# Optimization experiments

Hardware: AMD Instinct MI355X
Metric: run time of the kernel (lower is better)

The kernel has to match this reference:

```python
import jax, jax.numpy as jnp
import numpy as np

DIM = 1024
NUM_HEADS = 16
HEAD_DIM = DIM // NUM_HEADS
GATE_HID = DIM // 4


def setup_inputs() -> dict:
    key = jax.random.key(0)
    ks = jax.random.split(key, 16)
    B, S, D = 2, 2048, DIM
    sc = 1.0 / np.sqrt(D)
    inp = {
        "h": jax.random.normal(ks[0], (B, S, D), jnp.float32),
        "x": jax.random.normal(ks[1], (B, S, D), jnp.float32),
        # attention projections, stored (in, out) so y = x @ W + b
        "Wq": jax.random.normal(ks[2], (D, D), jnp.float32) * sc,
        "bq": jnp.zeros((D,), jnp.float32),
        "Wk": jax.random.normal(ks[3], (D, D), jnp.float32) * sc,
        "bk": jnp.zeros((D,), jnp.float32),
        "Wv": jax.random.normal(ks[4], (D, D), jnp.float32) * sc,
        "bv": jnp.zeros((D,), jnp.float32),
        "Wo": jax.random.normal(ks[5], (D, D), jnp.float32) * sc,
        "bo": jnp.zeros((D,), jnp.float32),
        # gating MLP: Linear(2D -> D//4) -> GELU -> Linear(D//4 -> D) -> sigmoid
        "Wg1": jax.random.normal(ks[6], (2 * D, GATE_HID), jnp.float32) * (1.0 / np.sqrt(2 * D)),
        "bg1": jnp.zeros((GATE_HID,), jnp.float32),
        "Wg2": jax.random.normal(ks[7], (GATE_HID, D), jnp.float32) * (1.0 / np.sqrt(GATE_HID)),
        "bg2": jnp.zeros((D,), jnp.float32),
    }
    return inp


def reference(h, x, Wq, bq, Wk, bk, Wv, bv, Wo, bo, Wg1, bg1, Wg2, bg2):
    B, S, D = h.shape
    # gated blend of latent h and input x
    gate_in = jnp.concatenate([h, x], axis=-1)                      # (B,S,2D)
    gate = jax.nn.sigmoid((jax.nn.gelu(gate_in @ Wg1 + bg1, approximate=False)) @ Wg2 + bg2)
    blended = gate * h + (1.0 - gate) * x                           # (B,S,D)
    # multi-head self-attention
    q = (blended @ Wq + bq).reshape(B, S, NUM_HEADS, HEAD_DIM)
    k = (blended @ Wk + bk).reshape(B, S, NUM_HEADS, HEAD_DIM)
    v = (blended @ Wv + bv).reshape(B, S, NUM_HEADS, HEAD_DIM)
    scale = 1.0 / np.sqrt(HEAD_DIM).astype(np.float32)
    scores = jnp.einsum('bqhd,bkhd->bhqk', q, k) * scale            # (B,H,S,S)
    attn = jax.nn.softmax(scores, axis=-1)
    out = jnp.einsum('bhqk,bkhd->bqhd', attn, v).reshape(B, S, D)
    return out @ Wo + bo
```

## Files before the change

kernel.cpp:

```cpp
#include <hip/hip_runtime.h>
#include <hip/hip_bf16.h>


typedef __attribute__((ext_vector_type(4))) unsigned int u32x4;
typedef __attribute__((ext_vector_type(8))) short s16x8;
typedef __attribute__((ext_vector_type(8))) unsigned short u16x8;
typedef __attribute__((ext_vector_type(4))) unsigned short u16x4;
typedef __attribute__((ext_vector_type(4))) float f32x4;

#define QSCALE 0.18033688011112043f
#define DEFER_THR 11.54f

__device__ __forceinline__ unsigned short f2bf(float f) {
    unsigned int i = __builtin_bit_cast(unsigned int, f);
    i += 0x7FFFu + ((i >> 16) & 1u);
    return (unsigned short)(i >> 16);
}

__device__ __forceinline__ void gload16(const void* g, void* l) {
    __builtin_amdgcn_global_load_lds(
        (const __attribute__((address_space(1))) void*)g,
        (__attribute__((address_space(3))) void*)l, 16, 0, 0);
}

struct TEntry { const float* src; unsigned short* dst; int K; int N; };
struct TTable { TEntry e[6]; };

__global__ __launch_bounds__(256) void transpose_cvt_all(TTable tt)
{
    const TEntry E = tt.e[blockIdx.y];
    const int ntn = E.N >> 5;
    if ((int)blockIdx.x >= (E.K >> 5) * ntn) return;
    const int n0 = ((int)blockIdx.x % ntn) * 32, k0 = ((int)blockIdx.x / ntn) * 32;
    __shared__ float tile[32][33];
    const int tx = threadIdx.x & 31, ty = threadIdx.x >> 5;
#pragma unroll
    for (int i = 0; i < 4; ++i)
        tile[ty + i * 8][tx] = E.src[(size_t)(k0 + ty + i * 8) * E.N + n0 + tx];
    __syncthreads();
#pragma unroll
    for (int i = 0; i < 4; ++i)
        E.dst[(size_t)(n0 + ty + i * 8) * E.K + k0 + tx] = f2bf(tile[tx][ty + i * 8]);
}

__global__ __launch_bounds__(256) void build_hx(
    const float* __restrict__ h, const float* __restrict__ x,
    unsigned short* __restrict__ hx)
{
    const int idx = blockIdx.x * 256 + threadIdx.x;
    const size_t e = (size_t)idx * 8;
    const int r = (int)(e >> 11), c = (int)(e & 2047);
    const float* src = (c < 1024) ? (h + (size_t)r * 1024 + c)
                                  : (x + (size_t)r * 1024 + (c - 1024));
    u16x8 o;
#pragma unroll
    for (int j = 0; j < 8; ++j) o[j] = f2bf(src[j]);
    *reinterpret_cast<u16x8*>(hx + e) = o;
}

__global__ __launch_bounds__(256) void concat_bias(
    const float* __restrict__ bq, const float* __restrict__ bk,
    const float* __restrict__ bv, float* __restrict__ dst)
{
    const int i = blockIdx.x * 256 + threadIdx.x;
    if (i < 1024) dst[i] = bq[i];
    else if (i < 2048) dst[i] = bk[i - 1024];
    else if (i < 3072) dst[i] = bv[i - 2048];
}

__global__ __launch_bounds__(256) void transpose_v(
    const unsigned short* __restrict__ qkv, unsigned short* __restrict__ vt)
{
    __shared__ unsigned short t[64][65];
    const int st = blockIdx.x;
    const int bh = blockIdx.y;
    const int b = bh >> 4, h = bh & 15;
    const int tx = threadIdx.x & 63, ty = threadIdx.x >> 6;
    const int s0 = st * 64;
    const size_t base = (size_t)(b * 2048 + s0) * 3072 + 2048 + h * 64;
#pragma unroll
    for (int i = 0; i < 16; ++i)
        t[ty + i * 4][tx] = qkv[base + (size_t)(ty + i * 4) * 3072 + tx];
    __syncthreads();
    const size_t obase = (size_t)(bh * 64) * 2048 + s0;
#pragma unroll
    for (int i = 0; i < 16; ++i)
        vt[obase + (size_t)(ty + i * 4) * 2048 + tx] = t[tx][ty + i * 4];
}

enum { EPI_GELU = 1, EPI_BLEND = 2, EPI_F32 = 3, EPI_QKV = 4 };

template <int EPI>
__global__ __launch_bounds__(256, 2) void gemm_kernel(
    const unsigned short* __restrict__ A, int lda,
    const unsigned short* __restrict__ Bt, int ldb,
    const float* __restrict__ bias,
    void* __restrict__ Cv, int ldc, int K,
    const float* __restrict__ hb, const float* __restrict__ xb,
    int swzn, int ntn)
{
    __shared__ unsigned short Alds[2][128 * 32];
    __shared__ unsigned short Blds[2][128 * 32];

    const int tid = threadIdx.x;
    const int lane = tid & 63;
    const int w = tid >> 6;
    const int wr = w >> 1, wc = w & 1;
    int mt, nt;
    if (swzn > 0) {
        const int xcd = (int)blockIdx.x & 7, seq = (int)blockIdx.x >> 3;
        nt = xcd * swzn + seq % swzn;
        mt = seq / swzn;
    } else {
        nt = (int)blockIdx.x % ntn;
        mt = (int)blockIdx.x / ntn;
    }
    const int m0 = mt * 128, n0 = nt * 128;
    const int lrow = lane & 15, lko = (lane >> 4) * 8;

    const int grow = w * 32 + (lane >> 2);
    const int gk8 = (lane & 3) * 8;
    const unsigned short* ga0 = A + (size_t)(m0 + grow) * lda + gk8;
    const unsigned short* ga1 = ga0 + (size_t)16 * lda;
    const unsigned short* gb0 = Bt + (size_t)(n0 + grow) * ldb + gk8;
    const unsigned short* gb1 = gb0 + (size_t)16 * ldb;

    auto stage = [&](int buf, int k0) {
        unsigned short* la = &Alds[buf][w * 1024];
        unsigned short* lb = &Blds[buf][w * 1024];
        gload16(ga0 + k0, la);
        gload16(ga1 + k0, la + 512);
        gload16(gb0 + k0, lb);
        gload16(gb1 + k0, lb + 512);
    };

    f32x4 acc[4][4];
#pragma unroll
    for (int i = 0; i < 4; ++i)
#pragma unroll
        for (int j = 0; j < 4; ++j) acc[i][j] = (f32x4){0.f, 0.f, 0.f, 0.f};

    const int kks = K >> 5;
    stage(0, 0);
    __syncthreads();

    for (int t = 0; t < kks; ++t) {
        const int cur = t & 1;
        if (t + 1 < kks) stage(cur ^ 1, (t + 1) << 5);

        s16x8 af[4], bfr[4];
#pragma unroll
        for (int mi = 0; mi < 4; ++mi)
            af[mi] = *reinterpret_cast<const s16x8*>(&Alds[cur][(wr * 64 + mi * 16 + lrow) * 32 + lko]);
#pragma unroll
        for (int ni = 0; ni < 4; ++ni)
            bfr[ni] = *reinterpret_cast<const s16x8*>(&Blds[cur][(wc * 64 + ni * 16 + lrow) * 32 + lko]);
#pragma unroll
        for (int mi = 0; mi < 4; ++mi)
#pragma unroll
            for (int ni = 0; ni < 4; ++ni)
                acc[mi][ni] = __builtin_amdgcn_mfma_f32_16x16x32_bf16(af[mi], bfr[ni], acc[mi][ni], 0, 0, 0);

        __syncthreads();
    }

    const int rbase = m0 + wr * 64;
    const int cbase = n0 + wc * 64;
#pragma unroll
    for (int mi = 0; mi < 4; ++mi) {
#pragma unroll
        for (int j = 0; j < 4; ++j) {
            const int r = rbase + mi * 16 + (lane >> 4) * 4 + j;
#pragma unroll
            for (int ni = 0; ni < 4; ++ni) {
                const int c = cbase + ni * 16 + (lane & 15);
                float v = acc[mi][ni][j] + bias[c];
                if constexpr (EPI == EPI_GELU) {
                    float g = 0.5f * v * (1.f + erff(v * 0.70710678118654752f));
                    ((unsigned short*)Cv)[(size_t)r * ldc + c] = f2bf(g);
                } else if constexpr (EPI == EPI_BLEND) {
                    float gate = 1.f / (1.f + __expf(-v));
                    const size_t o = (size_t)r * ldc + c;
                    float bl = gate * hb[o] + (1.f - gate) * xb[o];
                    ((unsigned short*)Cv)[o] = f2bf(bl);
                } else if constexpr (EPI == EPI_QKV) {
                    const float scl = (c < 1024) ? QSCALE : 1.f;
                    ((unsigned short*)Cv)[(size_t)r * ldc + c] = f2bf(v * scl);
                } else {
                    ((float*)Cv)[(size_t)r * ldc + c] = v;
                }
            }
        }
    }
}

__global__ __launch_bounds__(256, 2) void gemm_gelu64(
    const unsigned short* __restrict__ A, int lda,
    const unsigned short* __restrict__ Bt, int ldb,
    const float* __restrict__ bias,
    unsigned short* __restrict__ C, int ldc, int K)
{
    __shared__ unsigned short Alds[2][64 * 32];
    __shared__ unsigned short Blds[2][64 * 32];

    const int tid = threadIdx.x;
    const int lane = tid & 63;
    const int w = tid >> 6;
    const int wr = w >> 1, wc = w & 1;
    const int nt = (int)blockIdx.x & 3, mt = (int)blockIdx.x >> 2;
    const int m0 = mt * 64, n0 = nt * 64;
    const int lrow = lane & 15, lko = (lane >> 4) * 8;

    const int grow = w * 16 + (lane >> 2);
    const int gk8 = (lane & 3) * 8;
    const unsigned short* ga = A + (size_t)(m0 + grow) * lda + gk8;
    const unsigned short* gb = Bt + (size_t)(n0 + grow) * ldb + gk8;

    auto stage = [&](int buf, int k0) {
        gload16(ga + k0, &Alds[buf][w * 512]);
        gload16(gb + k0, &Blds[buf][w * 512]);
    };

    f32x4 acc[2][2];
#pragma unroll
    for (int i = 0; i < 2; ++i)
#pragma unroll
        for (int j = 0; j < 2; ++j) acc[i][j] = (f32x4){0.f, 0.f, 0.f, 0.f};

    const int kks = K >> 5;
    stage(0, 0);
    __syncthreads();

    for (int t = 0; t < kks; ++t) {
        const int cur = t & 1;
        if (t + 1 < kks) stage(cur ^ 1, (t + 1) << 5);

        s16x8 af[2], bfr[2];
#pragma unroll
        for (int mi = 0; mi < 2; ++mi)
            af[mi] = *reinterpret_cast<const s16x8*>(&Alds[cur][(wr * 32 + mi * 16 + lrow) * 32 + lko]);
#pragma unroll
        for (int ni = 0; ni < 2; ++ni)
            bfr[ni] = *reinterpret_cast<const s16x8*>(&Blds[cur][(wc * 32 + ni * 16 + lrow) * 32 + lko]);
#pragma unroll
        for (int mi = 0; mi < 2; ++mi)
#pragma unroll
            for (int ni = 0; ni < 2; ++ni)
                acc[mi][ni] = __builtin_amdgcn_mfma_f32_16x16x32_bf16(af[mi], bfr[ni], acc[mi][ni], 0, 0, 0);

        __syncthreads();
    }

    const int rbase = m0 + wr * 32;
    const int cbase = n0 + wc * 32;
#pragma unroll
    for (int mi = 0; mi < 2; ++mi) {
#pragma unroll
        for (int j = 0; j < 4; ++j) {
            const int r = rbase + mi * 16 + (lane >> 4) * 4 + j;
#pragma unroll
            for (int ni = 0; ni < 2; ++ni) {
                const int c = cbase + ni * 16 + (lane & 15);
                float v = acc[mi][ni][j] + bias[c];
                float g = 0.5f * v * (1.f + erff(v * 0.70710678118654752f));
                C[(size_t)r * ldc + c] = f2bf(g);
            }
        }
    }
}

#define ALD 72

__global__ __launch_bounds__(512, 4) void attn_kernel(
    const unsigned short* __restrict__ qkv,
    const unsigned short* __restrict__ vt,
    unsigned short* __restrict__ out)
{
    __shared__ unsigned short Klds[2][64 * ALD];
    __shared__ unsigned short Vlds[2][64 * ALD];
    __shared__ unsigned short Plds[8][16 * ALD];

    const int tid = threadIdx.x, lane = tid & 63, w = tid >> 6;
    const int xcd = (int)blockIdx.x & 7, seq = (int)blockIdx.x >> 3;
    const int bh = xcd * 4 + (seq & 3);
    const int qt = seq >> 2;
    const int b = bh >> 4, h = bh & 15;
    const int rb = b * 2048;
    const int lrow = lane & 15, g = lane >> 4, lko = g * 8;

    s16x8 qf[2];
    {
        const size_t qrow = (size_t)(rb + qt * 128 + w * 16 + lrow) * 3072 + h * 64;
        qf[0] = *reinterpret_cast<const s16x8*>(qkv + qrow + lko);
        qf[1] = *reinterpret_cast<const s16x8*>(qkv + qrow + 32 + lko);
    }

    const int srow = tid >> 3, sc8 = (tid & 7) * 8;
    const unsigned short* kp = qkv + (size_t)(rb + srow) * 3072 + 1024 + h * 64 + sc8;
    const unsigned short* vp = vt + (size_t)(bh * 64 + srow) * 2048 + sc8;

    u32x4 kreg, vreg;
    auto stage_load = [&](int t0) {
        kreg = *reinterpret_cast<const u32x4*>(kp + (size_t)t0 * 3072);
        vreg = *reinterpret_cast<const u32x4*>(vp + t0);
    };
    auto stage_write = [&](int buf) {
        *reinterpret_cast<u32x4*>(&Klds[buf][srow * ALD + sc8]) = kreg;
        *reinterpret_cast<u32x4*>(&Vlds[buf][srow * ALD + sc8]) = vreg;
    };

    f32x4 acc[4];
#pragma unroll
    for (int di = 0; di < 4; ++di) acc[di] = (f32x4){0.f, 0.f, 0.f, 0.f};
    float m = -INFINITY, lsum = 0.f;

    unsigned short* pw = &Plds[w][0];

    stage_load(0);
    stage_write(0);
    stage_load(64);
    __syncthreads();

    for (int t0 = 0; t0 < 2048; t0 += 64) {
        const int cur = (t0 >> 6) & 1;

        f32x4 s[4];
#pragma unroll
        for (int ni = 0; ni < 4; ++ni) s[ni] = (f32x4){0.f, 0.f, 0.f, 0.f};
#pragma unroll
        for (int ni = 0; ni < 4; ++ni)
#pragma unroll
            for (int fi = 0; fi < 2; ++fi) {
                s16x8 kf = *reinterpret_cast<const s16x8*>(&Klds[cur][(ni * 16 + lrow) * ALD + fi * 32 + lko]);
                s[ni] = __builtin_amdgcn_mfma_f32_16x16x32_bf16(kf, qf[fi], s[ni], 0, 0, 0);
            }

        if (t0 + 64 < 2048) stage_write(cur ^ 1);
        if (t0 + 128 < 2048) stage_load(t0 + 128);

        float pmax = -3.0e38f;
#pragma unroll
        for (int ni = 0; ni < 4; ++ni)
#pragma unroll
            for (int j = 0; j < 4; ++j) pmax = fmaxf(pmax, s[ni][j]);
        if (!__all(pmax <= m + DEFER_THR)) {
            float rm = fmaxf(pmax, __shfl_xor(pmax, 16));
            rm = fmaxf(rm, __shfl_xor(rm, 32));
            const float mnew = fmaxf(m, rm);
            const float alpha = __builtin_amdgcn_exp2f(m - mnew);
            m = mnew;
            lsum *= alpha;
#pragma unroll
            for (int di = 0; di < 4; ++di)
#pragma unroll
                for (int j = 0; j < 4; ++j) acc[di][j] *= alpha;
        }

        float ls = 0.f;
#pragma unroll
        for (int ni = 0; ni < 4; ++ni) {
            float p0 = __builtin_amdgcn_exp2f(s[ni][0] - m);
            float p1 = __builtin_amdgcn_exp2f(s[ni][1] - m);
            float p2 = __builtin_amdgcn_exp2f(s[ni][2] - m);
            float p3 = __builtin_amdgcn_exp2f(s[ni][3] - m);
            ls += (p0 + p1) + (p2 + p3);
            u16x4 pk = {f2bf(p0), f2bf(p1), f2bf(p2), f2bf(p3)};
            *reinterpret_cast<u16x4*>(&pw[lrow * ALD + ni * 16 + g * 4]) = pk;
        }
        ls += __shfl_xor(ls, 16);
        ls += __shfl_xor(ls, 32);
        lsum += ls;

#pragma unroll
        for (int st = 0; st < 2; ++st) {
            s16x8 pf = *reinterpret_cast<const s16x8*>(&pw[lrow * ALD + st * 32 + lko]);
#pragma unroll
            for (int di = 0; di < 4; ++di) {
                s16x8 vf = *reinterpret_cast<const s16x8*>(&Vlds[cur][(di * 16 + lrow) * ALD + st * 32 + lko]);
                acc[di] = __builtin_amdgcn_mfma_f32_16x16x32_bf16(vf, pf, acc[di], 0, 0, 0);
            }
        }

        __syncthreads();
    }

    const float inv = 1.f / lsum;
    const size_t orow = (size_t)(rb + qt * 128 + w * 16 + lrow) * 1024 + h * 64;
#pragma unroll
    for (int di = 0; di < 4; ++di) {
        u16x4 ov = {f2bf(acc[di][0] * inv), f2bf(acc[di][1] * inv),
                    f2bf(acc[di][2] * inv), f2bf(acc[di][3] * inv)};
        *reinterpret_cast<u16x4*>(&out[orow + di * 16 + g * 4]) = ov;
    }
}

extern "C" void kernel_launch(void* const* d_in, const int* in_sizes, int n_in,
                              void* d_out, int out_size, void* d_ws, size_t ws_size,
                              hipStream_t stream)
{
    const float* h   = (const float*)d_in[0];
    const float* x   = (const float*)d_in[1];
    const float* Wq  = (const float*)d_in[2];
    const float* bq  = (const float*)d_in[3];
    const float* Wk  = (const float*)d_in[4];
    const float* bk  = (const float*)d_in[5];
    const float* Wv  = (const float*)d_in[6];
    const float* bv  = (const float*)d_in[7];
    const float* Wo  = (const float*)d_in[8];
    const float* bo  = (const float*)d_in[9];
    const float* Wg1 = (const float*)d_in[10];
    const float* bg1 = (const float*)d_in[11];
    const float* Wg2 = (const float*)d_in[12];
    const float* bg2 = (const float*)d_in[13];

    char* ws = (char*)d_ws;
    size_t off = 0;
    auto alloc = [&](size_t bytes) {
        void* p = ws + off;
        off += (bytes + 255) & ~(size_t)255;
        return p;
    };
    unsigned short* wg1T  = (unsigned short*)alloc((size_t)256 * 2048 * 2);
    unsigned short* wg2T  = (unsigned short*)alloc((size_t)1024 * 256 * 2);
    unsigned short* wqkvT = (unsigned short*)alloc((size_t)3072 * 1024 * 2);
    unsigned short* woT   = (unsigned short*)alloc((size_t)1024 * 1024 * 2);
    float*          bqkv  = (float*)alloc((size_t)3072 * 4);
    unsigned short* blend = (unsigned short*)alloc((size_t)4096 * 1024 * 2);
    unsigned short* attno = (unsigned short*)alloc((size_t)4096 * 1024 * 2);
    unsigned short* vtb   = (unsigned short*)alloc((size_t)32 * 64 * 2048 * 2);
    char* uni = (char*)alloc((size_t)4096 * 3072 * 2);
    unsigned short* hx  = (unsigned short*)uni;
    unsigned short* g1  = (unsigned short*)(uni + (size_t)4096 * 2048 * 2);
    unsigned short* qkv = (unsigned short*)uni;
    (void)ws_size; (void)in_sizes; (void)n_in; (void)out_size;

    TTable tt;
    tt.e[0] = {Wg1, wg1T, 2048, 256};
    tt.e[1] = {Wg2, wg2T, 256, 1024};
    tt.e[2] = {Wq, wqkvT, 1024, 1024};
    tt.e[3] = {Wk, wqkvT + (size_t)1024 * 1024, 1024, 1024};
    tt.e[4] = {Wv, wqkvT + (size_t)2048 * 1024, 1024, 1024};
    tt.e[5] = {Wo, woT, 1024, 1024};
    transpose_cvt_all<<<dim3(1024, 6), 256, 0, stream>>>(tt);
    concat_bias<<<12, 256, 0, stream>>>(bq, bk, bv, bqkv);
    build_hx<<<4096, 256, 0, stream>>>(h, x, hx);

    gemm_gelu64<<<256, 256, 0, stream>>>(hx, 2048, wg1T, 2048, bg1, g1, 256, 2048);
    gemm_kernel<EPI_BLEND><<<256, 256, 0, stream>>>(
        g1, 256, wg2T, 256, bg2, blend, 1024, 256, h, x, 1, 8);

    gemm_kernel<EPI_QKV><<<768, 256, 0, stream>>>(
        blend, 1024, wqkvT, 1024, bqkv, qkv, 3072, 1024, nullptr, nullptr, 3, 24);

    transpose_v<<<dim3(32, 32), 256, 0, stream>>>(qkv, vtb);

    attn_kernel<<<512, 512, 0, stream>>>(qkv, vtb, attno);

    gemm_kernel<EPI_F32><<<256, 256, 0, stream>>>(
        attno, 1024, woT, 1024, bo, (float*)d_out, 1024, 1024, nullptr, nullptr, 1, 8);
}
```

Measured before the change: 183.6 us.

## Simplify bf16 rounding, pack pairs with perm, fold bias concat into build_hx

Replaces round-to-nearest-even bf16 conversion with a cheaper round-half-up and packs two bf16 values per 32-bit word using a byte-permute instruction in the attention softmax and output stores. The row-max reduction becomes a balanced tree. The separate bias-concatenation kernel is merged into build_hx as extra blocks, removing one launch. This cuts VALU work in the attention inner loop and some launch overhead, at the cost of slightly different rounding on ties.

```diff
diff --git a/kernel.cpp b/kernel.cpp
--- a/kernel.cpp
+++ b/kernel.cpp
@@ -3,6 +3,7 @@
 
 
 typedef __attribute__((ext_vector_type(4))) unsigned int u32x4;
+typedef __attribute__((ext_vector_type(2))) unsigned int u32x2;
 typedef __attribute__((ext_vector_type(8))) short s16x8;
 typedef __attribute__((ext_vector_type(8))) unsigned short u16x8;
 typedef __attribute__((ext_vector_type(4))) unsigned short u16x4;
@@ -12,9 +13,13 @@
 #define DEFER_THR 11.54f
 
 __device__ __forceinline__ unsigned short f2bf(float f) {
-    unsigned int i = __builtin_bit_cast(unsigned int, f);
-    i += 0x7FFFu + ((i >> 16) & 1u);
+    unsigned int i = __builtin_bit_cast(unsigned int, f) + 0x8000u;
     return (unsigned short)(i >> 16);
+}
+__device__ __forceinline__ unsigned int pack2bf(float a, float b) {
+    unsigned int ia = __builtin_bit_cast(unsigned int, a) + 0x8000u;
+    unsigned int ib = __builtin_bit_cast(unsigned int, b) + 0x8000u;
+    return __builtin_amdgcn_perm(ib, ia, 0x07060302u);
 }
 
 __device__ __forceinline__ void gload16(const void* g, void* l) {
@@ -45,8 +50,17 @@
 
 __global__ __launch_bounds__(256) void build_hx(
     const float* __restrict__ h, const float* __restrict__ x,
-    unsigned short* __restrict__ hx)
-{
+    unsigned short* __restrict__ hx,
+    const float* __restrict__ bq, const float* __restrict__ bk,
+    const float* __restrict__ bv, float* __restrict__ bqkv)
+{
+    if ((int)blockIdx.x >= 4096) {
+        const int i = ((int)blockIdx.x - 4096) * 256 + threadIdx.x;
+        if (i < 1024) bqkv[i] = bq[i];
+        else if (i < 2048) bqkv[i] = bk[i - 1024];
+        else if (i < 3072) bqkv[i] = bv[i - 2048];
+        return;
+    }
     const int idx = blockIdx.x * 256 + threadIdx.x;
     const size_t e = (size_t)idx * 8;
     const int r = (int)(e >> 11), c = (int)(e & 2047);
@@ -56,16 +70,6 @@
 #pragma unroll
     for (int j = 0; j < 8; ++j) o[j] = f2bf(src[j]);
     *reinterpret_cast<u16x8*>(hx + e) = o;
-}
-
-__global__ __launch_bounds__(256) void concat_bias(
-    const float* __restrict__ bq, const float* __restrict__ bk,
-    const float* __restrict__ bv, float* __restrict__ dst)
-{
-    const int i = blockIdx.x * 256 + threadIdx.x;
-    if (i < 1024) dst[i] = bq[i];
-    else if (i < 2048) dst[i] = bk[i - 1024];
-    else if (i < 3072) dst[i] = bv[i - 2048];
 }
 
 __global__ __launch_bounds__(256) void transpose_v(
@@ -338,11 +342,11 @@
         if (t0 + 64 < 2048) stage_write(cur ^ 1);
         if (t0 + 128 < 2048) stage_load(t0 + 128);
 
-        float pmax = -3.0e38f;
-#pragma unroll
-        for (int ni = 0; ni < 4; ++ni)
-#pragma unroll
-            for (int j = 0; j < 4; ++j) pmax = fmaxf(pmax, s[ni][j]);
+        float t01 = fmaxf(fmaxf(s[0][0], s[0][1]), fmaxf(s[0][2], s[0][3]));
+        float t23 = fmaxf(fmaxf(s[1][0], s[1][1]), fmaxf(s[1][2], s[1][3]));
+        float t45 = fmaxf(fmaxf(s[2][0], s[2][1]), fmaxf(s[2][2], s[2][3]));
+        float t67 = fmaxf(fmaxf(s[3][0], s[3][1]), fmaxf(s[3][2], s[3][3]));
+        float pmax = fmaxf(fmaxf(t01, t23), fmaxf(t45, t67));
         if (!__all(pmax <= m + DEFER_THR)) {
             float rm = fmaxf(pmax, __shfl_xor(pmax, 16));
             rm = fmaxf(rm, __shfl_xor(rm, 32));
@@ -364,8 +368,8 @@
             float p2 = __builtin_amdgcn_exp2f(s[ni][2] - m);
             float p3 = __builtin_amdgcn_exp2f(s[ni][3] - m);
             ls += (p0 + p1) + (p2 + p3);
-            u16x4 pk = {f2bf(p0), f2bf(p1), f2bf(p2), f2bf(p3)};
-            *reinterpret_cast<u16x4*>(&pw[lrow * ALD + ni * 16 + g * 4]) = pk;
+            u32x2 pk = {pack2bf(p0, p1), pack2bf(p2, p3)};
+            *reinterpret_cast<u32x2*>(&pw[lrow * ALD + ni * 16 + g * 4]) = pk;
         }
         ls += __shfl_xor(ls, 16);
         ls += __shfl_xor(ls, 32);
@@ -388,9 +392,9 @@
     const size_t orow = (size_t)(rb + qt * 128 + w * 16 + lrow) * 1024 + h * 64;
 #pragma unroll
     for (int di = 0; di < 4; ++di) {
-        u16x4 ov = {f2bf(acc[di][0] * inv), f2bf(acc[di][1] * inv),
-                    f2bf(acc[di][2] * inv), f2bf(acc[di][3] * inv)};
-        *reinterpret_cast<u16x4*>(&out[orow + di * 16 + g * 4]) = ov;
+        u32x2 ov = {pack2bf(acc[di][0] * inv, acc[di][1] * inv),
+                    pack2bf(acc[di][2] * inv, acc[di][3] * inv)};
+        *reinterpret_cast<u32x2*>(&out[orow + di * 16 + g * 4]) = ov;
     }
 }
 
@@ -442,8 +446,7 @@
     tt.e[4] = {Wv, wqkvT + (size_t)2048 * 1024, 1024, 1024};
     tt.e[5] = {Wo, woT, 1024, 1024};
     transpose_cvt_all<<<dim3(1024, 6), 256, 0, stream>>>(tt);
-    concat_bias<<<12, 256, 0, stream>>>(bq, bk, bv, bqkv);
-    build_hx<<<4096, 256, 0, stream>>>(h, x, hx);
+    build_hx<<<4108, 256, 0, stream>>>(h, x, hx, bq, bk, bv, bqkv);
 
     gemm_gelu64<<<256, 256, 0, stream>>>(hx, 2048, wg1T, 2048, bg1, g1, 256, 2048);
     gemm_kernel<EPI_BLEND><<<256, 256, 0, stream>>>(
```

After: 181.8 us. No clear change (-0.9%).
